# Performance work log

Hardware: AMD Instinct MI355X
Metric: run time of the kernel (lower is better)

Reference implementation:

```python
import jax, jax.numpy as jnp
import numpy as np

P = 16; D = 256; NH = 8; L = 4; E = 8; K = 2; B = 32; IMG = 224; NC = 1000; FF = 4 * D
N = (IMG // P) ** 2  # 196 patches
HD = D // NH  # head dim
EPS = 1e-5


def setup_inputs():
    key = jax.random.key(0)
    ks = iter(jax.random.split(key, 16))
    s = 0.02  # init scale keeps softmax/logits well-conditioned
    rn = lambda shape: jax.random.normal(next(ks), shape, jnp.float32) * s
    return dict(
        x=jax.random.normal(next(ks), (B, 3, IMG, IMG), jnp.float32),
        patch_w=rn((3 * P * P, D)), patch_b=jnp.zeros((D,), jnp.float32),
        cls_token=rn((1, 1, D)), pos_embed=rn((1, N + 1, D)),
        router_w=rn((L, D, E)), router_b=jnp.zeros((L, E), jnp.float32),
        ln1_g=jnp.ones((L, E, D), jnp.float32), ln1_b=jnp.zeros((L, E, D), jnp.float32),
        qkv_w=rn((L, E, D, 3 * D)), qkv_b=jnp.zeros((L, E, 3 * D), jnp.float32),
        proj_w=rn((L, E, D, D)), proj_b=jnp.zeros((L, E, D), jnp.float32),
        ln2_g=jnp.ones((L, E, D), jnp.float32), ln2_b=jnp.zeros((L, E, D), jnp.float32),
        fc1_w=rn((L, E, D, FF)), fc1_b=jnp.zeros((L, E, FF), jnp.float32),
        fc2_w=rn((L, E, FF, D)), fc2_b=jnp.zeros((L, E, D), jnp.float32),
        norm_g=jnp.ones((D,), jnp.float32), norm_b=jnp.zeros((D,), jnp.float32),
        head_w=rn((D, NC)), head_b=jnp.zeros((NC,), jnp.float32),
    )


def _ln(x, g, b):
    m = x.mean(-1, keepdims=True)
    v = ((x - m) ** 2).mean(-1, keepdims=True)
    return (x - m) * jax.lax.rsqrt(v + EPS) * g + b


def _block(x, g1, b1, wqkv, bqkv, wp, bp, g2, b2, w1, bias1, w2, bias2):
    # standard ViT block: LN -> MHA -> residual, LN -> MLP(GELU) -> residual
    bsz, S, _ = x.shape
    h = _ln(x, g1, b1)
    qkv = (h @ wqkv + bqkv).reshape(bsz, S, 3, NH, HD)
    q, k, v = qkv[:, :, 0], qkv[:, :, 1], qkv[:, :, 2]  # [B,S,NH,HD]
    scores = jnp.einsum('bqhd,bkhd->bhqk', q, k) / np.float32(np.sqrt(HD))
    attn = jax.nn.softmax(scores, axis=-1)
    o = jnp.einsum('bhqk,bkhd->bqhd', attn, v).reshape(bsz, S, D)
    x = x + o @ wp + bp
    h2 = _ln(x, g2, b2)
    x = x + jax.nn.gelu(h2 @ w1 + bias1, approximate=False) @ w2 + bias2
    return x


def _moe_layer(x, rw, rb, g1, b1, wqkv, bqkv, wp, bp, g2, b2, w1, bias1, w2, bias2):
    probs = jax.nn.softmax(x @ rw + rb, axis=-1)            # [B,S,E]
    topv, topi = jax.lax.top_k(probs, K)                    # [B,S,K]
    topv = topv / topv.sum(-1, keepdims=True)
    # dense all-expert compute (faithful to source), vmapped over experts
    eo = jax.vmap(_block, in_axes=(None,) + (0,) * 12)(
        x, g1, b1, wqkv, bqkv, wp, bp, g2, b2, w1, bias1, w2, bias2)  # [E,B,S,D]
    eo = jnp.moveaxis(eo, 0, 2)                             # [B,S,E,D]
    sel = jnp.take_along_axis(eo, topi[..., None], axis=2)  # [B,S,K,D]
    return (sel * topv[..., None]).sum(axis=2)


def reference(x, patch_w, patch_b, cls_token, pos_embed, router_w, router_b,
              ln1_g, ln1_b, qkv_w, qkv_b, proj_w, proj_b, ln2_g, ln2_b,
              fc1_w, fc1_b, fc2_w, fc2_b, norm_g, norm_b, head_w, head_b):
    bsz = x.shape[0]
    g = IMG // P
    # patch embed: stride==kernel conv == patch extraction + matmul
    patches = x.reshape(bsz, 3, g, P, g, P).transpose(0, 2, 4, 1, 3, 5).reshape(bsz, N, 3 * P * P)
    h = patches @ patch_w + patch_b                          # [B,N,D]
    cls = jnp.broadcast_to(cls_token, (bsz, 1, D))
    h = jnp.concatenate([cls, h], axis=1) + pos_embed        # [B,N+1,D]
    for l in range(L):
        h = _moe_layer(h, router_w[l], router_b[l], ln1_g[l], ln1_b[l],
                       qkv_w[l], qkv_b[l], proj_w[l], proj_b[l], ln2_g[l], ln2_b[l],
                       fc1_w[l], fc1_b[l], fc2_w[l], fc2_b[l])
    h = _ln(h, norm_g, norm_b)
    return h[:, 0] @ head_w + head_b                         # [B,NC]
```

## Files before the change

### kernel.cpp

```cpp
#include <hip/hip_runtime.h>
#include <math.h>

#define SEQ 197
#define BATCH 32
#define DIM 256
#define NHEAD 8
#define HDIM 32
#define NEXP 8
#define NLAYER 4
#define FFDIM 1024
#define NCLS 1000
#define NPATCH 196
#define TOK (BATCH * SEQ)
#define CAP 13120
#define YB 99

__global__ __launch_bounds__(256) void k_im2col(const float* __restrict__ x,
                                                float* __restrict__ Apat) {
  int idx = blockIdx.x * 256 + threadIdx.x;
  if (idx >= BATCH * NPATCH * 768) return;
  int cpp = idx % 768;
  int m = idx / 768;
  int n = m % NPATCH;
  int b = m / NPATCH;
  int c = cpp >> 8;
  int py = (cpp >> 4) & 15;
  int px = cpp & 15;
  int gy = n / 14, gx = n % 14;
  Apat[idx] = x[(((size_t)b * 3 + c) * 224 + gy * 16 + py) * 224 + gx * 16 + px];
}

template <bool AFF>
__global__ __launch_bounds__(256) void k_gemm_t(
    const float* __restrict__ A, const float* __restrict__ W,
    const float* __restrict__ bias, const float* __restrict__ gsc,
    const float* __restrict__ gof, const float* __restrict__ R,
    const float* __restrict__ X2, const float* __restrict__ PW,
    const int* __restrict__ ptok, const int* __restrict__ off_e,
    const int* __restrict__ cnt_e, float* __restrict__ out, int M, int N,
    int K, int Wld, int wcol, int bstride, int ebase, int mode, int flags) {
  __shared__ float As[16][68];
  __shared__ float Bs[16][132];
  int ez = blockIdx.z;
  int e = ebase + ez;
  bool seg = (flags & 1) != 0;
  int rows = seg ? cnt_e[e] : M;
  int row0 = blockIdx.y * 64;
  if (row0 >= rows) return;
  int col0 = blockIdx.x * 128;
  int tid = threadIdx.x;
  int base = seg ? off_e[e] : 0;
  const float* Wp = W + (size_t)e * K * Wld + wcol;
  const float* bp = bias + (size_t)e * bstride + wcol;

  int rr = tid >> 2, kq = (tid & 3) * 4;
  int r = row0 + rr;
  bool val = r < rows;
  int rc = val ? r : rows - 1;
  int gr0 = base + rc;
  int arow = seg ? ((flags & 2) ? ptok[gr0] : gr0) : rc;
  const float* aptr = A + (size_t)arow * K + kq;
  float msk = val ? 1.f : 0.f;
  const float* gptr = AFF ? gsc + (size_t)e * K + kq : nullptr;
  const float* optr = AFF ? gof + (size_t)e * K + kq : nullptr;
  int bk = tid >> 5;
  int bc = (tid & 31) * 4;
  const float* bptr = Wp + (size_t)bk * Wld + col0 + bc;

  int tx = tid & 15, ty = tid >> 4;
  float acc0[4][4] = {};
  float acc1[4][4] = {};
  for (int k0 = 0; k0 < K; k0 += 16) {
    float4 av = *(const float4*)(aptr + k0);
    if (AFF) {
      float4 gv = *(const float4*)(gptr + k0);
      float4 ov = *(const float4*)(optr + k0);
      av.x = fmaf(av.x, gv.x, ov.x);
      av.y = fmaf(av.y, gv.y, ov.y);
      av.z = fmaf(av.z, gv.z, ov.z);
      av.w = fmaf(av.w, gv.w, ov.w);
    }
    As[kq + 0][rr] = av.x * msk;
    As[kq + 1][rr] = av.y * msk;
    As[kq + 2][rr] = av.z * msk;
    As[kq + 3][rr] = av.w * msk;
    const float* bt = bptr + (size_t)k0 * Wld;
    *(float4*)&Bs[bk][bc] = *(const float4*)bt;
    *(float4*)&Bs[bk + 8][bc] = *(const float4*)(bt + (size_t)8 * Wld);
    __syncthreads();
#pragma unroll
    for (int k = 0; k < 16; ++k) {
      float4 a = *(const float4*)&As[k][ty * 4];
      float4 b0 = *(const float4*)&Bs[k][tx * 4];
      float4 b1 = *(const float4*)&Bs[k][64 + tx * 4];
      float aa[4] = {a.x, a.y, a.z, a.w};
      float b0a[4] = {b0.x, b0.y, b0.z, b0.w};
      float b1a[4] = {b1.x, b1.y, b1.z, b1.w};
#pragma unroll
      for (int i = 0; i < 4; ++i) {
#pragma unroll
        for (int j = 0; j < 4; ++j) {
          acc0[i][j] = fmaf(aa[i], b0a[j], acc0[i][j]);
          acc1[i][j] = fmaf(aa[i], b1a[j], acc1[i][j]);
        }
      }
    }
    __syncthreads();
  }
#pragma unroll
  for (int i = 0; i < 4; ++i) {
    int rrow = row0 + ty * 4 + i;
    if (rrow >= rows) continue;
    int gr = base + rrow;
#pragma unroll
    for (int c = 0; c < 2; ++c) {
#pragma unroll
      for (int j = 0; j < 4; ++j) {
        int col = col0 + c * 64 + tx * 4 + j;
        float v = (c ? acc1[i][j] : acc0[i][j]) + bp[col];
        if (mode == 0) {
          size_t orow = seg ? (size_t)gr : (size_t)ez * M + rrow;
          out[orow * N + col] = v;
        } else if (mode == 1) {
          int t = ptok[gr];
          out[(size_t)gr * N + col] = v + R[(size_t)t * N + col];
        } else if (mode == 2) {
          out[(size_t)gr * N + col] =
              0.5f * v * (1.f + erff(v * 0.70710678118654752f));
        } else {
          int t = ptok[gr];
          atomicAdd(&out[(size_t)t * N + col],
                    PW[gr] * (X2[(size_t)gr * N + col] + v));
        }
      }
    }
  }
}

__global__ __launch_bounds__(256) void k_assemble(const float* __restrict__ tmp,
                                                  const float* __restrict__ cls,
                                                  const float* __restrict__ pos,
                                                  float* __restrict__ h) {
  int idx = blockIdx.x * 256 + threadIdx.x;
  if (idx >= TOK * DIM) return;
  int d = idx & 255;
  int t = idx >> 8;
  int s = t % SEQ;
  int b = t / SEQ;
  float v = (s == 0) ? cls[d] : tmp[((size_t)b * NPATCH + s - 1) * DIM + d];
  h[idx] = v + pos[s * DIM + d];
}

__global__ __launch_bounds__(64) void k_router(
    const float* __restrict__ h, const float* __restrict__ rw,
    const float* __restrict__ rb, int* __restrict__ cnt_eb,
    int* __restrict__ tmp_s, float* __restrict__ tmp_w) {
  int t = blockIdx.x;
  int lane = threadIdx.x;
  float hv[4];
  const float* hp = h + (size_t)t * DIM + lane * 4;
#pragma unroll
  for (int i = 0; i < 4; i++) hv[i] = hp[i];
  float lg[8];
#pragma unroll
  for (int e = 0; e < 8; e++) {
    float p = 0.f;
#pragma unroll
    for (int i = 0; i < 4; i++) p = fmaf(hv[i], rw[(lane * 4 + i) * 8 + e], p);
#pragma unroll
    for (int off = 32; off; off >>= 1) p += __shfl_down(p, off);
    lg[e] = p;
  }
  if (lane == 0) {
#pragma unroll
    for (int e = 0; e < 8; e++) lg[e] += rb[e];
    float mx = lg[0];
#pragma unroll
    for (int e = 1; e < 8; e++) mx = fmaxf(mx, lg[e]);
    float pr[8];
#pragma unroll
    for (int e = 0; e < 8; e++) pr[e] = expf(lg[e] - mx);
    int i0 = 0;
#pragma unroll
    for (int e = 1; e < 8; e++)
      if (pr[e] > pr[i0]) i0 = e;
    int i1 = -1;
#pragma unroll
    for (int e = 0; e < 8; e++)
      if (e != i0 && (i1 < 0 || pr[e] > pr[i1])) i1 = e;
    float wsum = pr[i0] + pr[i1];
    int b = t / SEQ, s = t - b * SEQ;
    int eb0 = i0 * 32 + b;
    int p0 = atomicAdd(&cnt_eb[eb0], 1);
    tmp_s[eb0 * SEQ + p0] = s;
    tmp_w[eb0 * SEQ + p0] = pr[i0] / wsum;
    int eb1 = i1 * 32 + b;
    int p1 = atomicAdd(&cnt_eb[eb1], 1);
    tmp_s[eb1 * SEQ + p1] = s;
    tmp_w[eb1 * SEQ + p1] = pr[i1] / wsum;
  }
}

__global__ __launch_bounds__(64) void k_scan(const int* __restrict__ cnt_eb,
                                             int* __restrict__ off_eb,
                                             int* __restrict__ off_e,
                                             int* __restrict__ cnt_e) {
  if (threadIdx.x == 0 && blockIdx.x == 0) {
    int g = 0;
    for (int e = 0; e < 8; e++) {
      off_e[e] = g;
      int ce = 0;
      for (int b = 0; b < 32; b++) {
        off_eb[e * 32 + b] = g + ce;
        ce += cnt_eb[e * 32 + b];
      }
      cnt_e[e] = ce;
      g += (ce + 63) & ~63;
    }
  }
}

__global__ __launch_bounds__(256) void k_scatter(
    const int* __restrict__ cnt_eb, const int* __restrict__ off_eb,
    const int* __restrict__ tmp_s, const float* __restrict__ tmp_w,
    int* __restrict__ ptok, float* __restrict__ pw) {
  int eb = blockIdx.x;
  int b = eb & 31;
  int c = cnt_eb[eb];
  int o = off_eb[eb];
  for (int i = threadIdx.x; i < c; i += 256) {
    ptok[o + i] = b * SEQ + tmp_s[eb * SEQ + i];
    pw[o + i] = tmp_w[eb * SEQ + i];
  }
}

__global__ __launch_bounds__(256) void k_ln_noaff(const float* __restrict__ X,
                                                  float* __restrict__ Y) {
  int t = blockIdx.x;
  int d = threadIdx.x;
  float v = X[(size_t)t * DIM + d];
  __shared__ float red[4];
  float s = v;
#pragma unroll
  for (int o = 32; o; o >>= 1) s += __shfl_down(s, o);
  if ((d & 63) == 0) red[d >> 6] = s;
  __syncthreads();
  float mean = (red[0] + red[1] + red[2] + red[3]) * (1.f / 256.f);
  __syncthreads();
  float c = v - mean;
  float s2 = c * c;
#pragma unroll
  for (int o = 32; o; o >>= 1) s2 += __shfl_down(s2, o);
  if ((d & 63) == 0) red[d >> 6] = s2;
  __syncthreads();
  float var = (red[0] + red[1] + red[2] + red[3]) * (1.f / 256.f);
  Y[(size_t)t * DIM + d] = c * rsqrtf(var + 1e-5f);
}

__global__ __launch_bounds__(256) void k_ln_seg(
    const float* __restrict__ X, const float* __restrict__ g,
    const float* __restrict__ bta, float* __restrict__ Y,
    const int* __restrict__ off_e, const int* __restrict__ cnt_e) {
  int e = blockIdx.y;
  int cnt = cnt_e[e];
  int base = off_e[e];
  int d = threadIdx.x;
  float gv = g[e * DIM + d];
  float bv = bta[e * DIM + d];
  __shared__ float red[4];
  for (int r = blockIdx.x; r < cnt; r += gridDim.x) {
    size_t gr = (size_t)(base + r);
    float v = X[gr * DIM + d];
    float s = v;
#pragma unroll
    for (int o = 32; o; o >>= 1) s += __shfl_down(s, o);
    if ((d & 63) == 0) red[d >> 6] = s;
    __syncthreads();
    float mean = (red[0] + red[1] + red[2] + red[3]) * (1.f / 256.f);
    __syncthreads();
    float c = v - mean;
    float s2 = c * c;
#pragma unroll
    for (int o = 32; o; o >>= 1) s2 += __shfl_down(s2, o);
    if ((d & 63) == 0) red[d >> 6] = s2;
    __syncthreads();
    float var = (red[0] + red[1] + red[2] + red[3]) * (1.f / 256.f);
    Y[gr * DIM + d] = c * rsqrtf(var + 1e-5f) * gv + bv;
    __syncthreads();
  }
}

__global__ __launch_bounds__(256) void k_attn(
    const float* __restrict__ qc, const float* __restrict__ kv,
    float* __restrict__ oc, const int* __restrict__ cnt_eb,
    const int* __restrict__ off_eb, int ebase) {
  int bx = blockIdx.x;
  int hh = bx & 7;
  int b = (bx >> 3) & 31;
  int ez = bx >> 8;
  int eb = (ebase + ez) * 32 + b;
  int cnt = cnt_eb[eb];
  if (cnt == 0) return;
  int off = off_eb[eb];
  __shared__ float Ks[SEQ][HDIM];
  __shared__ float Vs[SEQ][HDIM];
  const float* base = kv + ((size_t)ez * TOK + (size_t)b * SEQ) * 512;
  int tid = threadIdx.x;
  for (int i = tid; i < SEQ * 8; i += 256) {
    int row = i >> 3, c4 = (i & 7) * 4;
    const float* kp = base + (size_t)row * 512 + hh * HDIM + c4;
    *(float4*)&Ks[row][c4] = *(const float4*)kp;
    *(float4*)&Vs[row][c4] = *(const float4*)(kp + 256);
  }
  __syncthreads();
  int q = tid;
  if (q >= cnt) return;
  float qv[HDIM];
  const float* qp = qc + (size_t)(off + q) * DIM + hh * HDIM;
#pragma unroll
  for (int i = 0; i < 8; i++) {
    float4 t = *(const float4*)(qp + i * 4);
    qv[i * 4 + 0] = t.x;
    qv[i * 4 + 1] = t.y;
    qv[i * 4 + 2] = t.z;
    qv[i * 4 + 3] = t.w;
  }
  float m = -1e30f, l = 0.f;
  float acc[HDIM] = {};
  for (int j = 0; j < SEQ; ++j) {
    float s = 0.f;
#pragma unroll
    for (int d = 0; d < HDIM; ++d) s = fmaf(qv[d], Ks[j][d], s);
    s *= 0.17677669529663687f;
    float e2;
    if (s > m) {
      float f = expf(m - s);
      l *= f;
#pragma unroll
      for (int d = 0; d < HDIM; ++d) acc[d] *= f;
      m = s;
      e2 = 1.f;
    } else {
      e2 = expf(s - m);
    }
    l += e2;
#pragma unroll
    for (int d = 0; d < HDIM; ++d) acc[d] = fmaf(e2, Vs[j][d], acc[d]);
  }
  float inv = 1.f / l;
  float* op = oc + (size_t)(off + q) * DIM + hh * HDIM;
#pragma unroll
  for (int i = 0; i < 8; i++) {
    float4 t;
    t.x = acc[i * 4 + 0] * inv;
    t.y = acc[i * 4 + 1] * inv;
    t.z = acc[i * 4 + 2] * inv;
    t.w = acc[i * 4 + 3] * inv;
    *(float4*)(op + i * 4) = t;
  }
}

__global__ __launch_bounds__(256) void k_head(const float* __restrict__ h,
                                              const float* __restrict__ ng,
                                              const float* __restrict__ nb,
                                              const float* __restrict__ hw,
                                              const float* __restrict__ hb,
                                              float* __restrict__ out) {
  int b = blockIdx.x;
  int d = threadIdx.x;
  float v = h[(size_t)b * SEQ * DIM + d];
  __shared__ float red[4];
  __shared__ float hls[DIM];
  float s = v;
#pragma unroll
  for (int off = 32; off; off >>= 1) s += __shfl_down(s, off);
  if ((d & 63) == 0) red[d >> 6] = s;
  __syncthreads();
  float mean = (red[0] + red[1] + red[2] + red[3]) * (1.f / 256.f);
  __syncthreads();
  float c = v - mean;
  float s2 = c * c;
#pragma unroll
  for (int off = 32; off; off >>= 1) s2 += __shfl_down(s2, off);
  if ((d & 63) == 0) red[d >> 6] = s2;
  __syncthreads();
  float var = (red[0] + red[1] + red[2] + red[3]) * (1.f / 256.f);
  hls[d] = c * rsqrtf(var + 1e-5f) * ng[d] + nb[d];
  __syncthreads();
  for (int j = d; j < NCLS; j += 256) {
    float sdot = hb[j];
    for (int k2 = 0; k2 < DIM; k2++)
      sdot = fmaf(hls[k2], hw[(size_t)k2 * NCLS + j], sdot);
    out[(size_t)b * NCLS + j] = sdot;
  }
}

extern "C" void kernel_launch(void* const* d_in, const int* in_sizes, int n_in,
                              void* d_out, int out_size, void* d_ws,
                              size_t ws_size, hipStream_t stream) {
  const float* x = (const float*)d_in[0];
  const float* patch_w = (const float*)d_in[1];
  const float* patch_b = (const float*)d_in[2];
  const float* cls_token = (const float*)d_in[3];
  const float* pos_embed = (const float*)d_in[4];
  const float* router_w = (const float*)d_in[5];
  const float* router_b = (const float*)d_in[6];
  const float* ln1_g = (const float*)d_in[7];
  const float* ln1_b = (const float*)d_in[8];
  const float* qkv_w = (const float*)d_in[9];
  const float* qkv_b = (const float*)d_in[10];
  const float* proj_w = (const float*)d_in[11];
  const float* proj_b = (const float*)d_in[12];
  const float* ln2_g = (const float*)d_in[13];
  const float* ln2_b = (const float*)d_in[14];
  const float* fc1_w = (const float*)d_in[15];
  const float* fc1_b = (const float*)d_in[16];
  const float* fc2_w = (const float*)d_in[17];
  const float* fc2_b = (const float*)d_in[18];
  const float* norm_g = (const float*)d_in[19];
  const float* norm_b = (const float*)d_in[20];
  const float* head_w = (const float*)d_in[21];
  const float* head_b = (const float*)d_in[22];

  float* ws = (float*)d_ws;
  size_t off = 0;
  float* xhat = ws + off; off += (size_t)TOK * DIM;
  float* hbuf = ws + off; off += (size_t)TOK * DIM;
  float* accb = ws + off; off += (size_t)TOK * DIM;
  float* qc   = ws + off; off += (size_t)CAP * DIM;
  float* oc   = ws + off; off += (size_t)CAP * DIM;
  float* x2c  = ws + off; off += (size_t)CAP * DIM;
  float* ffc  = ws + off; off += (size_t)CAP * FFDIM;
  float* pwb  = ws + off; off += CAP;
  float* tmpw = ws + off; off += 256 * SEQ;
  int* ptok   = (int*)(ws + off); off += CAP;
  int* tmps   = (int*)(ws + off); off += 256 * SEQ;
  int* cnt_eb = (int*)(ws + off); off += 256;
  int* off_eb = (int*)(ws + off); off += 256;
  int* off_e  = (int*)(ws + off); off += 8;
  int* cnt_e  = (int*)(ws + off); off += 8;
  float* kv4 = ffc;
  float* hlnc = qc;

  int tot = BATCH * NPATCH * 768;
  k_im2col<<<(tot + 255) / 256, 256, 0, stream>>>(x, ffc);
  k_gemm_t<false><<<dim3(2, 98, 1), 256, 0, stream>>>(
      ffc, patch_w, patch_b, nullptr, nullptr, nullptr, nullptr, nullptr,
      nullptr, nullptr, nullptr, qc, BATCH * NPATCH, DIM, 768, DIM, 0, 0, 0, 0,
      0);
  k_assemble<<<(TOK * DIM + 255) / 256, 256, 0, stream>>>(qc, cls_token,
                                                          pos_embed, hbuf);

  float* h = hbuf;
  float* acc = accb;
  for (int l = 0; l < NLAYER; ++l) {
    hipMemsetAsync(acc, 0, (size_t)TOK * DIM * sizeof(float), stream);
    hipMemsetAsync(cnt_eb, 0, 256 * sizeof(int), stream);
    k_router<<<TOK, 64, 0, stream>>>(h, router_w + (size_t)l * DIM * NEXP,
                                     router_b + (size_t)l * NEXP, cnt_eb, tmps,
                                     tmpw);
    k_scan<<<1, 64, 0, stream>>>(cnt_eb, off_eb, off_e, cnt_e);
    k_scatter<<<256, 256, 0, stream>>>(cnt_eb, off_eb, tmps, tmpw, ptok, pwb);
    k_ln_noaff<<<TOK, 256, 0, stream>>>(h, xhat);

    const float* g1 = ln1_g + (size_t)l * NEXP * DIM;
    const float* b1 = ln1_b + (size_t)l * NEXP * DIM;
    const float* Wqkv = qkv_w + (size_t)l * NEXP * DIM * 768;
    const float* Bqkv = qkv_b + (size_t)l * NEXP * 768;

    k_gemm_t<true><<<dim3(2, YB, 8), 256, 0, stream>>>(
        xhat, Wqkv, Bqkv, g1, b1, nullptr, nullptr, nullptr, ptok, off_e,
        cnt_e, qc, 0, DIM, DIM, 768, 0, 768, 0, 0, 3);

    for (int grp = 0; grp < 2; ++grp) {
      int eb0 = grp * 4;
      k_gemm_t<true><<<dim3(4, YB, 4), 256, 0, stream>>>(
          xhat, Wqkv, Bqkv, g1, b1, nullptr, nullptr, nullptr, nullptr,
          nullptr, nullptr, kv4, TOK, 512, DIM, 768, 256, 768, eb0, 0, 0);
      k_attn<<<1024, 256, 0, stream>>>(qc, kv4, oc, cnt_eb, off_eb, eb0);
    }

    k_gemm_t<false><<<dim3(2, YB, 8), 256, 0, stream>>>(
        oc, proj_w + (size_t)l * NEXP * DIM * DIM,
        proj_b + (size_t)l * NEXP * DIM, nullptr, nullptr, h, nullptr, nullptr,
        ptok, off_e, cnt_e, x2c, 0, DIM, DIM, DIM, 0, DIM, 0, 1, 1);
    k_ln_seg<<<dim3(YB, 8), 256, 0, stream>>>(
        x2c, ln2_g + (size_t)l * NEXP * DIM, ln2_b + (size_t)l * NEXP * DIM,
        hlnc, off_e, cnt_e);
    k_gemm_t<false><<<dim3(8, YB, 8), 256, 0, stream>>>(
        hlnc, fc1_w + (size_t)l * NEXP * DIM * FFDIM,
        fc1_b + (size_t)l * NEXP * FFDIM, nullptr, nullptr, nullptr, nullptr,
        nullptr, ptok, off_e, cnt_e, ffc, 0, FFDIM, DIM, FFDIM, 0, FFDIM, 0, 2,
        1);
    k_gemm_t<false><<<dim3(2, YB, 8), 256, 0, stream>>>(
        ffc, fc2_w + (size_t)l * NEXP * FFDIM * DIM,
        fc2_b + (size_t)l * NEXP * DIM, nullptr, nullptr, nullptr, x2c, pwb,
        ptok, off_e, cnt_e, acc, 0, DIM, FFDIM, DIM, 0, DIM, 0, 3, 1);
    float* t = h;
    h = acc;
    acc = t;
  }
  k_head<<<BATCH, 256, 0, stream>>>(h, norm_g, norm_b, head_w, head_b,
                                    (float*)d_out);
}
```

Before: 3.748 ms.

## Double-buffer GEMM tiles with direct-to-LDS loads, fold LN1 affine, remap XCDs

The GEMM kernel now double-buffers its A and B shared-memory tiles and loads the weight tile with global_load_lds straight into LDS, prefetching the next k-slice while the current one is computed. This halves the barriers per k-step. The LN1 gain and bias are folded once into the QKV weights and bias by two new prologue kernels, which removes the per-element affine from the A-tile load. Block indices are also remapped so consecutive tiles land on the same XCD for better L2 reuse. The costs are a larger weight workspace and an extra pass over all QKV weights each call.

```diff
diff --git a/kernel.cpp b/kernel.cpp
--- a/kernel.cpp
+++ b/kernel.cpp
@@ -15,6 +15,12 @@
 #define CAP 13120
 #define YB 99
 
+__device__ __forceinline__ void gload16(const float* g, float* l) {
+  __builtin_amdgcn_global_load_lds(
+      (const __attribute__((address_space(1))) void*)g,
+      (__attribute__((address_space(3))) void*)l, 16, 0, 0);
+}
+
 __global__ __launch_bounds__(256) void k_im2col(const float* __restrict__ x,
                                                 float* __restrict__ Apat) {
   int idx = blockIdx.x * 256 + threadIdx.x;
@@ -30,24 +36,56 @@
   Apat[idx] = x[(((size_t)b * 3 + c) * 224 + gy * 16 + py) * 224 + gx * 16 + px];
 }
 
-template <bool AFF>
+__global__ __launch_bounds__(256) void k_foldw(const float* __restrict__ qw,
+                                               const float* __restrict__ g1,
+                                               float* __restrict__ w4) {
+  size_t idx = (size_t)blockIdx.x * 256 + threadIdx.x;
+  if (idx >= (size_t)32 * 256 * 768) return;
+  size_t kn = idx % (256 * 768);
+  int le = (int)(idx / (256 * 768));
+  int k = (int)(kn / 768);
+  w4[idx] = qw[idx] * g1[le * 256 + k];
+}
+
+__global__ __launch_bounds__(256) void k_foldb(const float* __restrict__ qw,
+                                               const float* __restrict__ qb,
+                                               const float* __restrict__ b1,
+                                               float* __restrict__ b4) {
+  int le = blockIdx.y;
+  int col = blockIdx.x * 256 + threadIdx.x;
+  const float* w = qw + (size_t)le * 256 * 768 + col;
+  const float* lb = b1 + (size_t)le * 256;
+  float acc = 0.f;
+  for (int k = 0; k < 256; ++k) acc = fmaf(lb[k], w[(size_t)k * 768], acc);
+  b4[(size_t)le * 768 + col] = acc + qb[(size_t)le * 768 + col];
+}
+
 __global__ __launch_bounds__(256) void k_gemm_t(
     const float* __restrict__ A, const float* __restrict__ W,
-    const float* __restrict__ bias, const float* __restrict__ gsc,
-    const float* __restrict__ gof, const float* __restrict__ R,
+    const float* __restrict__ bias, const float* __restrict__ R,
     const float* __restrict__ X2, const float* __restrict__ PW,
     const int* __restrict__ ptok, const int* __restrict__ off_e,
     const int* __restrict__ cnt_e, float* __restrict__ out, int M, int N,
     int K, int Wld, int wcol, int bstride, int ebase, int mode, int flags) {
-  __shared__ float As[16][68];
-  __shared__ float Bs[16][132];
-  int ez = blockIdx.z;
-  int e = ebase + ez;
+  __shared__ float As[2][16][68];
+  __shared__ float Bs[2][16][128];
+  int gx = gridDim.x, gy = gridDim.y;
+  int nwg = gx * gy * gridDim.z;
+  int lin = blockIdx.x + gx * (blockIdx.y + gy * blockIdx.z);
+  int q8 = nwg >> 3, r8 = nwg & 7;
+  int xcd = lin & 7, jj0 = lin >> 3;
+  int nlin = (xcd < r8 ? xcd * (q8 + 1) : r8 * (q8 + 1) + (xcd - r8) * q8) + jj0;
+  int bx = nlin % gx;
+  int t1 = nlin / gx;
+  int by = t1 % gy;
+  int bz = t1 / gy;
+
+  int e = ebase + bz;
   bool seg = (flags & 1) != 0;
   int rows = seg ? cnt_e[e] : M;
-  int row0 = blockIdx.y * 64;
+  int row0 = by * 64;
   if (row0 >= rows) return;
-  int col0 = blockIdx.x * 128;
+  int col0 = bx * 128;
   int tid = threadIdx.x;
   int base = seg ? off_e[e] : 0;
   const float* Wp = W + (size_t)e * K * Wld + wcol;
@@ -61,51 +99,59 @@
   int arow = seg ? ((flags & 2) ? ptok[gr0] : gr0) : rc;
   const float* aptr = A + (size_t)arow * K + kq;
   float msk = val ? 1.f : 0.f;
-  const float* gptr = AFF ? gsc + (size_t)e * K + kq : nullptr;
-  const float* optr = AFF ? gof + (size_t)e * K + kq : nullptr;
-  int bk = tid >> 5;
-  int bc = (tid & 31) * 4;
-  const float* bptr = Wp + (size_t)bk * Wld + col0 + bc;
+  int wv = tid >> 6, lane = tid & 63;
+  const float* bsrc0 =
+      Wp + (size_t)(2 * wv + (lane >> 5)) * Wld + col0 + (lane & 31) * 4;
+  const float* bsrc1 = bsrc0 + (size_t)8 * Wld;
+
+  gload16(bsrc0, &Bs[0][2 * wv][0]);
+  gload16(bsrc1, &Bs[0][8 + 2 * wv][0]);
+  {
+    float4 av = *(const float4*)aptr;
+    As[0][kq + 0][rr] = av.x * msk;
+    As[0][kq + 1][rr] = av.y * msk;
+    As[0][kq + 2][rr] = av.z * msk;
+    As[0][kq + 3][rr] = av.w * msk;
+  }
+  __syncthreads();
 
   int tx = tid & 15, ty = tid >> 4;
   float acc0[4][4] = {};
   float acc1[4][4] = {};
+  int cur = 0;
   for (int k0 = 0; k0 < K; k0 += 16) {
-    float4 av = *(const float4*)(aptr + k0);
-    if (AFF) {
-      float4 gv = *(const float4*)(gptr + k0);
-      float4 ov = *(const float4*)(optr + k0);
-      av.x = fmaf(av.x, gv.x, ov.x);
-      av.y = fmaf(av.y, gv.y, ov.y);
-      av.z = fmaf(av.z, gv.z, ov.z);
-      av.w = fmaf(av.w, gv.w, ov.w);
-    }
-    As[kq + 0][rr] = av.x * msk;
-    As[kq + 1][rr] = av.y * msk;
-    As[kq + 2][rr] = av.z * msk;
-    As[kq + 3][rr] = av.w * msk;
-    const float* bt = bptr + (size_t)k0 * Wld;
-    *(float4*)&Bs[bk][bc] = *(const float4*)bt;
-    *(float4*)&Bs[bk + 8][bc] = *(const float4*)(bt + (size_t)8 * Wld);
-    __syncthreads();
+    int nb = cur ^ 1;
+    bool more = (k0 + 16) < K;
+    float4 av;
+    if (more) {
+      av = *(const float4*)(aptr + k0 + 16);
+      gload16(bsrc0 + (size_t)(k0 + 16) * Wld, &Bs[nb][2 * wv][0]);
+      gload16(bsrc1 + (size_t)(k0 + 16) * Wld, &Bs[nb][8 + 2 * wv][0]);
+    }
 #pragma unroll
     for (int k = 0; k < 16; ++k) {
-      float4 a = *(const float4*)&As[k][ty * 4];
-      float4 b0 = *(const float4*)&Bs[k][tx * 4];
-      float4 b1 = *(const float4*)&Bs[k][64 + tx * 4];
+      float4 a = *(const float4*)&As[cur][k][ty * 4];
+      float4 b0 = *(const float4*)&Bs[cur][k][tx * 4];
+      float4 b1 = *(const float4*)&Bs[cur][k][64 + tx * 4];
       float aa[4] = {a.x, a.y, a.z, a.w};
       float b0a[4] = {b0.x, b0.y, b0.z, b0.w};
       float b1a[4] = {b1.x, b1.y, b1.z, b1.w};
 #pragma unroll
-      for (int i = 0; i < 4; ++i) {
+      for (int i = 0; i < 4; ++i)
 #pragma unroll
         for (int j = 0; j < 4; ++j) {
           acc0[i][j] = fmaf(aa[i], b0a[j], acc0[i][j]);
           acc1[i][j] = fmaf(aa[i], b1a[j], acc1[i][j]);
         }
-      }
+    }
+    if (more) {
+      As[nb][kq + 0][rr] = av.x * msk;
+      As[nb][kq + 1][rr] = av.y * msk;
+      As[nb][kq + 2][rr] = av.z * msk;
+      As[nb][kq + 3][rr] = av.w * msk;
     }
     __syncthreads();
+    cur = nb;
   }
 #pragma unroll
   for (int i = 0; i < 4; ++i) {
@@ -119,7 +165,7 @@
         int col = col0 + c * 64 + tx * 4 + j;
         float v = (c ? acc1[i][j] : acc0[i][j]) + bp[col];
         if (mode == 0) {
-          size_t orow = seg ? (size_t)gr : (size_t)ez * M + rrow;
+          size_t orow = seg ? (size_t)gr : (size_t)bz * M + rrow;
           out[orow * N + col] = v;
         } else if (mode == 1) {
           int t = ptok[gr];
@@ -431,6 +477,8 @@
   float* oc   = ws + off; off += (size_t)CAP * DIM;
   float* x2c  = ws + off; off += (size_t)CAP * DIM;
   float* ffc  = ws + off; off += (size_t)CAP * FFDIM;
+  float* w4   = ws + off; off += (size_t)32 * DIM * 768;
+  float* b4   = ws + off; off += (size_t)32 * 768;
   float* pwb  = ws + off; off += CAP;
   float* tmpw = ws + off; off += 256 * SEQ;
   int* ptok   = (int*)(ws + off); off += CAP;
@@ -442,12 +490,14 @@
   float* kv4 = ffc;
   float* hlnc = qc;
 
+  k_foldw<<<(32 * 256 * 768 + 255) / 256, 256, 0, stream>>>(qkv_w, ln1_g, w4);
+  k_foldb<<<dim3(3, 32), 256, 0, stream>>>(qkv_w, qkv_b, ln1_b, b4);
+
   int tot = BATCH * NPATCH * 768;
   k_im2col<<<(tot + 255) / 256, 256, 0, stream>>>(x, ffc);
-  k_gemm_t<false><<<dim3(2, 98, 1), 256, 0, stream>>>(
+  k_gemm_t<<<dim3(2, 98, 1), 256, 0, stream>>>(
       ffc, patch_w, patch_b, nullptr, nullptr, nullptr, nullptr, nullptr,
-      nullptr, nullptr, nullptr, qc, BATCH * NPATCH, DIM, 768, DIM, 0, 0, 0, 0,
-      0);
+      nullptr, qc, BATCH * NPATCH, DIM, 768, DIM, 0, 0, 0, 0, 0);
   k_assemble<<<(TOK * DIM + 255) / 256, 256, 0, stream>>>(qc, cls_token,
                                                           pos_embed, hbuf);
 
@@ -463,39 +513,36 @@
     k_scatter<<<256, 256, 0, stream>>>(cnt_eb, off_eb, tmps, tmpw, ptok, pwb);
     k_ln_noaff<<<TOK, 256, 0, stream>>>(h, xhat);
 
-    const float* g1 = ln1_g + (size_t)l * NEXP * DIM;
-    const float* b1 = ln1_b + (size_t)l * NEXP * DIM;
-    const float* Wqkv = qkv_w + (size_t)l * NEXP * DIM * 768;
-    const float* Bqkv = qkv_b + (size_t)l * NEXP * 768;
-
-    k_gemm_t<true><<<dim3(2, YB, 8), 256, 0, stream>>>(
-        xhat, Wqkv, Bqkv, g1, b1, nullptr, nullptr, nullptr, ptok, off_e,
-        cnt_e, qc, 0, DIM, DIM, 768, 0, 768, 0, 0, 3);
+    const float* Wl = w4 + (size_t)l * NEXP * DIM * 768;
+    const float* Bl = b4 + (size_t)l * NEXP * 768;
+
+    k_gemm_t<<<dim3(2, YB, 8), 256, 0, stream>>>(
+        xhat, Wl, Bl, nullptr, nullptr, nullptr, ptok, off_e, cnt_e, qc, 0,
+        DIM, DIM, 768, 0, 768, 0, 0, 3);
 
     for (int grp = 0; grp < 2; ++grp) {
       int eb0 = grp * 4;
-      k_gemm_t<true><<<dim3(4, YB, 4), 256, 0, stream>>>(
-          xhat, Wqkv, Bqkv, g1, b1, nullptr, nullptr, nullptr, nullptr,
-          nullptr, nullptr, kv4, TOK, 512, DIM, 768, 256, 768, eb0, 0, 0);
+      k_gemm_t<<<dim3(4, YB, 4), 256, 0, stream>>>(
+          xhat, Wl, Bl, nullptr, nullptr, nullptr, nullptr, nullptr, nullptr,
+          kv4, TOK, 512, DIM, 768, 256, 768, eb0, 0, 0);
       k_attn<<<1024, 256, 0, stream>>>(qc, kv4, oc, cnt_eb, off_eb, eb0);
     }
 
-    k_gemm_t<false><<<dim3(2, YB, 8), 256, 0, stream>>>(
+    k_gemm_t<<<dim3(2, YB, 8), 256, 0, stream>>>(
         oc, proj_w + (size_t)l * NEXP * DIM * DIM,
-        proj_b + (size_t)l * NEXP * DIM, nullptr, nullptr, h, nullptr, nullptr,
-        ptok, off_e, cnt_e, x2c, 0, DIM, DIM, DIM, 0, DIM, 0, 1, 1);
+        proj_b + (size_t)l * NEXP * DIM, h, nullptr, nullptr, ptok, off_e,
+        cnt_e, x2c, 0, DIM, DIM, DIM, 0, DIM, 0, 1, 1);
     k_ln_seg<<<dim3(YB, 8), 256, 0, stream>>>(
         x2c, ln2_g + (size_t)l * NEXP * DIM, ln2_b + (size_t)l * NEXP * DIM,
         hlnc, off_e, cnt_e);
-    k_gemm_t<false><<<dim3(8, YB, 8), 256, 0, stream>>>(
+    k_gemm_t<<<dim3(8, YB, 8), 256, 0, stream>>>(
         hlnc, fc1_w + (size_t)l * NEXP * DIM * FFDIM,
-        fc1_b + (size_t)l * NEXP * FFDIM, nullptr, nullptr, nullptr, nullptr,
-        nullptr, ptok, off_e, cnt_e, ffc, 0, FFDIM, DIM, FFDIM, 0, FFDIM, 0, 2,
-        1);
-    k_gemm_t<false><<<dim3(2, YB, 8), 256, 0, stream>>>(
+        fc1_b + (size_t)l * NEXP * FFDIM, nullptr, nullptr, nullptr, ptok,
+        off_e, cnt_e, ffc, 0, FFDIM, DIM, FFDIM, 0, FFDIM, 0, 2, 1);
+    k_gemm_t<<<dim3(2, YB, 8), 256, 0, stream>>>(
         ffc, fc2_w + (size_t)l * NEXP * FFDIM * DIM,
-        fc2_b + (size_t)l * NEXP * DIM, nullptr, nullptr, nullptr, x2c, pwb,
-        ptok, off_e, cnt_e, acc, 0, DIM, FFDIM, DIM, 0, DIM, 0, 3, 1);
+        fc2_b + (size_t)l * NEXP * DIM, nullptr, x2c, pwb, ptok, off_e, cnt_e,
+        acc, 0, DIM, FFDIM, DIM, 0, DIM, 0, 3, 1);
     float* t = h;
     h = acc;
     acc = t;
```

Result: no change. 3.789 ms (+1.1%).
